# Optimization experiments

Measured on AMD Instinct MI355X. Metric: run time of the kernel, lower is better.

The kernel has to match this reference:

```python
import jax, jax.numpy as jnp
import numpy as np

B, S, E = 2, 2048, 4096
HQ, HKV, D = 32, 8, 128
WINDOW = 1024
SOFT_CAP = 50.0
Q_PRE_ATTN = 128.0
TT_SCALE = 0.1
TT_FLOOR = 8192.0
EPS = 1e-6
ROPE_BASE = 10000.0


def l2norm(x):
    return x * jax.lax.rsqrt(jnp.mean(x * x, axis=-1, keepdims=True) + EPS)


def apply_rope(x, pos):
    # x: [B,S,H,D]; half-split rotary, base 10000
    half = x.shape[-1] // 2
    freq = ROPE_BASE ** (-jnp.arange(half, dtype=jnp.float32) * 2.0 / x.shape[-1])  # [half]
    angle = pos.astype(jnp.float32)[:, None] * freq[None, :]                         # [S,half]
    cos = jnp.cos(angle)[None, :, None, :]
    sin = jnp.sin(angle)[None, :, None, :]
    x1, x2 = x[..., :half], x[..., half:]
    return jnp.concatenate([x1 * cos - x2 * sin, x2 * cos + x1 * sin], axis=-1)


def setup_inputs() -> dict:
    key = jax.random.key(0)
    ks = jax.random.split(key, 5)
    sc = 0.02
    return {
        "x": jax.random.normal(ks[0], (B, S, E), jnp.float32),
        "Wq": jax.random.normal(ks[1], (E, HQ, D), jnp.float32) * sc,
        "Wk": jax.random.normal(ks[2], (E, HKV, D), jnp.float32) * sc,
        "Wv": jax.random.normal(ks[3], (E, HKV, D), jnp.float32) * sc,
        "Wo": jax.random.normal(ks[4], (HQ, D, E), jnp.float32) * sc,
    }


def reference(x, Wq, Wk, Wv, Wo):
    pos = jnp.arange(S)
    # QKV projections
    q = jnp.einsum('bse,ehd->bshd', x, Wq)   # [B,S,HQ,D]
    k = jnp.einsum('bse,ehd->bshd', x, Wk)   # [B,S,HKV,D]
    v = jnp.einsum('bse,ehd->bshd', x, Wv)   # [B,S,HKV,D]
    # QK norm (L2Norm) then RoPE
    q = apply_rope(l2norm(q), pos)
    k = apply_rope(l2norm(k), pos)
    # query pre-attention scaling
    q = q * (Q_PRE_ATTN ** -0.5)
    # temperature tuning: per-position scale
    attn_scale = jnp.log(jnp.floor((pos.astype(jnp.float32) + 1.0) / TT_FLOOR) + 1.0) * TT_SCALE + 1.0
    q = q * attn_scale[None, :, None, None]
    # GQA: expand kv heads
    g = HQ // HKV
    k_r = jnp.repeat(k, g, axis=2)           # [B,S,HQ,D]
    v_r = jnp.repeat(v, g, axis=2)
    logits = jnp.einsum('bihd,bjhd->bhij', q, k_r).astype(jnp.float32)
    # tanh soft cap
    logits = SOFT_CAP * jnp.tanh(logits / SOFT_CAP)
    # causal + sliding window mask: j <= i and i - j < WINDOW
    i = pos[:, None]
    j = pos[None, :]
    mask = (j <= i) & ((i - j) < WINDOW)     # [S,S]
    logits = jnp.where(mask[None, None], logits, jnp.float32(-1e30))
    probs = jax.nn.softmax(logits, axis=-1)
    out = jnp.einsum('bhij,bjhd->bihd', probs, v_r)  # [B,S,HQ,D]
    return jnp.einsum('bihd,hde->bie', out, Wo)      # [B,S,E]
```

## Files before the change

### kernel.cpp

```cpp
#include <hip/hip_runtime.h>


typedef unsigned short u16;
typedef unsigned int   u32;
typedef __bf16 bf16x8 __attribute__((ext_vector_type(8)));
typedef float  f32x4  __attribute__((ext_vector_type(4)));

typedef __attribute__((address_space(1))) void* gas_ptr;
typedef __attribute__((address_space(3))) void* las_ptr;

__device__ __forceinline__ void load_lds16(const void* g, void* l) {
  __builtin_amdgcn_global_load_lds((gas_ptr)g, (las_ptr)l, 16, 0, 0);
}

__device__ __forceinline__ u16 f2bf(float f) {
  u32 u = __builtin_bit_cast(u32, f);
  u += 0x7fffu + ((u >> 16) & 1u);
  return (u16)(u >> 16);
}
__device__ __forceinline__ float bf2f(u16 h) {
  u32 u = ((u32)h) << 16;
  return __builtin_bit_cast(float, u);
}
__device__ __forceinline__ u32 pack_trunc(float a, float b) {
  return (__builtin_bit_cast(u32, a) >> 16) | (__builtin_bit_cast(u32, b) & 0xffff0000u);
}

__global__ __launch_bounds__(256) void cast_f32_bf16(const float* __restrict__ src,
                                                     u16* __restrict__ dst) {
  size_t i = ((size_t)blockIdx.x * 256 + threadIdx.x) * 8;
  float4 a = *(const float4*)(src + i);
  float4 b = *(const float4*)(src + i + 4);
  uint4 o;
  o.x = (u32)f2bf(a.x) | ((u32)f2bf(a.y) << 16);
  o.y = (u32)f2bf(a.z) | ((u32)f2bf(a.w) << 16);
  o.z = (u32)f2bf(b.x) | ((u32)f2bf(b.y) << 16);
  o.w = (u32)f2bf(b.z) | ((u32)f2bf(b.w) << 16);
  *(uint4*)(dst + i) = o;
}

__global__ __launch_bounds__(256) void transpose_cast_f32_bf16(
    const float* __restrict__ src, u16* __restrict__ dst, int R, int C) {
  __shared__ float tile[32][33];
  const int tx = threadIdx.x & 31, ty = threadIdx.x >> 5;
  const int r0 = blockIdx.y * 32, c0 = blockIdx.x * 32;
#pragma unroll
  for (int i = 0; i < 4; ++i)
    tile[ty + i * 8][tx] = src[(size_t)(r0 + ty + i * 8) * C + (c0 + tx)];
  __syncthreads();
  uint2 ov;
  ov.x = (u32)f2bf(tile[ty * 4 + 0][tx]) | ((u32)f2bf(tile[ty * 4 + 1][tx]) << 16);
  ov.y = (u32)f2bf(tile[ty * 4 + 2][tx]) | ((u32)f2bf(tile[ty * 4 + 3][tx]) << 16);
  *(uint2*)&dst[(size_t)(c0 + tx) * R + (r0 + ty * 4)] = ov;
}

__global__ __launch_bounds__(256) void transpose_v(const u16* __restrict__ qkvr,
                                                   u16* __restrict__ vtb) {
  __shared__ u16 tile[32][34];
  const int plane = blockIdx.z;
  const int b = plane >> 3, h8 = plane & 7;
  const u16* s = qkvr + (size_t)(b * 2048) * 6144 + (40 + h8) * 128;
  u16* d = vtb + (size_t)plane * 2048 * 128;
  const int tx = threadIdx.x & 31, ty = threadIdx.x >> 5;
  const int r0 = blockIdx.x * 32, c0 = blockIdx.y * 32;
#pragma unroll
  for (int i = 0; i < 4; ++i)
    tile[ty + i * 8][tx] = s[(size_t)(r0 + ty + i * 8) * 6144 + (c0 + tx)];
  __syncthreads();
  uint2 ov;
  ov.x = (u32)tile[ty * 4 + 0][tx] | ((u32)tile[ty * 4 + 1][tx] << 16);
  ov.y = (u32)tile[ty * 4 + 2][tx] | ((u32)tile[ty * 4 + 3][tx] << 16);
  *(uint2*)&d[(size_t)(c0 + tx) * 2048 + (r0 + ty * 4)] = ov;
}


template <int MB>
__device__ __forceinline__ void mm16(f32x4 (&acc)[8][4], const bf16x8 (&af)[4],
                                     const bf16x8 (&bf)[4]) {
#pragma unroll
  for (int ii = 0; ii < 4; ++ii)
#pragma unroll
    for (int nf = 0; nf < 4; ++nf)
      acc[MB + ii][nf] =
          __builtin_amdgcn_mfma_f32_16x16x32_bf16(af[ii], bf[nf], acc[MB + ii][nf], 0, 0, 0);
}

template <int OUT_BF16>
__global__ __launch_bounds__(512, 2) void gemm256(const u16* __restrict__ A,
                                                  const u16* __restrict__ Bt,
                                                  void* __restrict__ Cout,
                                                  int N, int K, int ntx) {
  __shared__ __align__(16) u16 lds[65536];
  const int t = threadIdx.x, lane = t & 63, w = t >> 6;
  const int c = lane & 15, q = lane >> 4;
  const int wm = w >> 2, wn = w & 3;

  const int cpx = (int)gridDim.x >> 3;
  const int swz = ((int)blockIdx.x & 7) * cpx + ((int)blockIdx.x >> 3);
  const int bx = swz % ntx, by = swz / ntx;
  const int m0 = by << 8, n0 = bx << 8;

  u32 aoff[2][2], boff[2][2];
#pragma unroll
  for (int h = 0; h < 2; ++h)
#pragma unroll
    for (int j = 0; j < 2; ++j) {
      const int rowS = w * 16 + j * 8 + (lane >> 3);
      const int colE = ((lane & 7) ^ (rowS & 7)) * 8;
      aoff[h][j] = (u32)(m0 + h * 128 + rowS) * (u32)K + (u32)colE;
      boff[h][j] = (u32)(n0 + h * 128 + rowS) * (u32)K + (u32)colE;
    }
  const u32 stW = (u32)w * 1024u;

  const u32 sl0 = (u32)((q ^ (c & 7)) * 8);
  const u32 aR = (u32)(wm * 8192 + c * 64) + sl0;
  const u32 bR = (u32)(16384 + (wn >> 1) * 8192 + (wn & 1) * 4096 + c * 64) + sl0;

  f32x4 acc[8][4];
#pragma unroll
  for (int i2 = 0; i2 < 8; ++i2)
#pragma unroll
    for (int j2 = 0; j2 < 4; ++j2) acc[i2][j2] = (f32x4){0.f, 0.f, 0.f, 0.f};

  const int nt = K >> 6;

#define STG_A(bb, hh, kt)                                                \
  do {                                                                   \
    u16* d_ = &lds[(bb) * 32768u + (hh) * 8192u + stW];                  \
    load_lds16(A + (aoff[hh][0] + (u32)(kt) * 64u), d_);                 \
    load_lds16(A + (aoff[hh][1] + (u32)(kt) * 64u), d_ + 512);           \
  } while (0)
#define STG_B(bb, hh, kt)                                                \
  do {                                                                   \
    u16* d_ = &lds[(bb) * 32768u + 16384u + (hh) * 8192u + stW];         \
    load_lds16(Bt + (boff[hh][0] + (u32)(kt) * 64u), d_);                \
    load_lds16(Bt + (boff[hh][1] + (u32)(kt) * 64u), d_ + 512);          \
  } while (0)
#define RD4(dst, base)                                                   \
  do {                                                                   \
    const u16* p_ = &lds[(base)];                                        \
    dst[0] = *(const bf16x8*)(p_);                                       \
    dst[1] = *(const bf16x8*)(p_ + 1024);                                \
    dst[2] = *(const bf16x8*)(p_ + 2048);                                \
    dst[3] = *(const bf16x8*)(p_ + 3072);                                \
  } while (0)
#define BAR __builtin_amdgcn_s_barrier()
#define LGKM0 asm volatile("s_waitcnt lgkmcnt(0)" ::: "memory")
#define LGKM8 asm volatile("s_waitcnt lgkmcnt(8)" ::: "memory")
#define VM6 asm volatile("s_waitcnt vmcnt(6)" ::: "memory")
#define PRIO1 __builtin_amdgcn_s_setprio(1)
#define PRIO0 __builtin_amdgcn_s_setprio(0)

  STG_B(0, 0, 0);
  STG_B(0, 1, 0);
  STG_A(0, 0, 0);
  STG_A(0, 1, 0);
  STG_B(1, 0, 1);
  STG_B(1, 1, 1);
  STG_A(1, 0, 1);
  VM6;
  BAR;

  bf16x8 Bf0[4], Bf1[4], Af0[4], Af1[4];

  for (int i = 0; i < (nt >> 1); ++i) {
    const int tb = 2 * i + 1;
    int t2 = 2 * i + 2; if (t2 >= nt) t2 -= nt;
    int t3 = 2 * i + 3; if (t3 >= nt) t3 -= nt;

    RD4(Bf0, bR);
    RD4(Bf1, bR ^ 32u);
    RD4(Af0, aR);
    STG_A(1, 1, tb);
    LGKM8;
    BAR; LGKM0;
    PRIO1; mm16<0>(acc, Af0, Bf0); PRIO0;
    BAR;
    RD4(Af1, aR + 4096u);
    STG_B(0, 0, t2);
    BAR; LGKM0;
    PRIO1; mm16<4>(acc, Af1, Bf0); PRIO0;
    BAR;
    RD4(Af0, aR ^ 32u);
    RD4(Af1, (aR + 4096u) ^ 32u);
    STG_B(0, 1, t2);
    BAR; LGKM0;
    PRIO1; mm16<0>(acc, Af0, Bf1); PRIO0;
    BAR;
    STG_A(0, 0, t2);
    VM6;
    BAR;
    PRIO1; mm16<4>(acc, Af1, Bf1); PRIO0;
    BAR;

    RD4(Bf0, 32768u + bR);
    RD4(Bf1, (32768u + bR) ^ 32u);
    RD4(Af0, 32768u + aR);
    STG_A(0, 1, t2);
    LGKM8;
    BAR; LGKM0;
    PRIO1; mm16<0>(acc, Af0, Bf0); PRIO0;
    BAR;
    RD4(Af1, 32768u + aR + 4096u);
    STG_B(1, 0, t3);
    BAR; LGKM0;
    PRIO1; mm16<4>(acc, Af1, Bf0); PRIO0;
    BAR;
    RD4(Af0, (32768u + aR) ^ 32u);
    RD4(Af1, (32768u + aR + 4096u) ^ 32u);
    STG_B(1, 1, t3);
    BAR; LGKM0;
    PRIO1; mm16<0>(acc, Af0, Bf1); PRIO0;
    BAR;
    STG_A(1, 0, t3);
    VM6;
    BAR;
    PRIO1; mm16<4>(acc, Af1, Bf1); PRIO0;
    BAR;
  }

  asm volatile("s_waitcnt vmcnt(0)" ::: "memory");

#undef STG_A
#undef STG_B
#undef RD4
#undef BAR
#undef LGKM0
#undef LGKM8
#undef VM6
#undef PRIO1
#undef PRIO0

  const int rb0 = m0 + wm * 128 + q * 4;
  const int cb0 = n0 + wn * 64 + c;
#pragma unroll
  for (int mf = 0; mf < 8; ++mf)
#pragma unroll
    for (int nf = 0; nf < 4; ++nf) {
      const size_t base = (size_t)(rb0 + mf * 16) * N + (cb0 + nf * 16);
#pragma unroll
      for (int r = 0; r < 4; ++r) {
        if (OUT_BF16)
          ((u16*)Cout)[base + (size_t)r * N] = f2bf(acc[mf][nf][r]);
        else
          ((float*)Cout)[base + (size_t)r * N] = acc[mf][nf][r];
      }
    }
}

__global__ __launch_bounds__(256) void qkv_post(const u16* __restrict__ raw,
                                                u16* __restrict__ qb,
                                                u16* __restrict__ kb) {
  const int t = threadIdx.x;
  const int c = t & 15, g = t >> 4;
  const u32 u = (u32)blockIdx.x * 16u + (u32)g;
  const u32 row = u / 40u;
  const int hh = (int)(u - row * 40u);
  const int pos = (int)(row & 2047u);
  const int b = (int)(row >> 11);

  const uint4 rv = *(const uint4*)(raw + (size_t)row * 6144 + hh * 128 + c * 8);
  u32 rw[4] = {rv.x, rv.y, rv.z, rv.w};
  float xs[8];
#pragma unroll
  for (int j = 0; j < 4; ++j) {
    xs[2 * j] = bf2f((u16)(rw[j] & 0xffffu));
    xs[2 * j + 1] = bf2f((u16)(rw[j] >> 16));
  }
  float ss = 0.f;
#pragma unroll
  for (int j = 0; j < 8; ++j) ss += xs[j] * xs[j];
#pragma unroll
  for (int off = 8; off >= 1; off >>= 1) ss += __shfl_xor(ss, off);
  const float rn = rsqrtf(ss * (1.0f / 128.0f) + 1e-6f);

  u32 pw[4];
#pragma unroll
  for (int j = 0; j < 4; ++j) pw[j] = __shfl_xor(rw[j], 8);
  float xp[8];
#pragma unroll
  for (int j = 0; j < 4; ++j) {
    xp[2 * j] = bf2f((u16)(pw[j] & 0xffffu));
    xp[2 * j + 1] = bf2f((u16)(pw[j] >> 16));
  }

  const float sgn = (c < 8) ? -1.0f : 1.0f;
  const int dbase = (c & 7) * 8;
  const float fpos = (float)pos;
  const bool isq = (hh < 32);
  const float sc = (isq ? 0.088388347648318447f : 1.0f) * rn;
  float o[8];
#pragma unroll
  for (int j = 0; j < 8; ++j) {
    const float fr = exp2f(-(float)(dbase + j) * 0.20762050593046f);
    float sn, cs;
    sincosf(fpos * fr, &sn, &cs);
    o[j] = (xs[j] * cs + sgn * xp[j] * sn) * sc;
  }

  uint4 ov;
  ov.x = (u32)f2bf(o[0]) | ((u32)f2bf(o[1]) << 16);
  ov.y = (u32)f2bf(o[2]) | ((u32)f2bf(o[3]) << 16);
  ov.z = (u32)f2bf(o[4]) | ((u32)f2bf(o[5]) << 16);
  ov.w = (u32)f2bf(o[6]) | ((u32)f2bf(o[7]) << 16);
  u16* dst = isq ? (qb + ((size_t)((b * 32 + hh) * 2048 + pos)) * 128)
                 : (kb + ((size_t)((b * 8 + (hh - 32)) * 2048 + pos)) * 128);
  *(uint4*)(dst + c * 8) = ov;
}

__global__ __launch_bounds__(256, 4) void attn_fwd(const u16* __restrict__ qb,
                                                   const u16* __restrict__ kb,
                                                   const u16* __restrict__ vtb,
                                                   u16* __restrict__ attn) {
  __shared__ __align__(16) u16 Ks[64 * 128];
  __shared__ __align__(16) u16 VTs[128 * 64];
  __shared__ __align__(16) u16 Ps[4][16 * 64];

  const int t = threadIdx.x, lane = t & 63, w = t >> 6;
  const int c = lane & 15, quad = lane >> 4;
  const int q0 = blockIdx.x * 64;
  const int bh = blockIdx.y;
  const int b = bh >> 5, hq = bh & 31;
  const int kvp = b * 8 + (hq >> 2);
  const u16* qp = qb + (size_t)bh * (2048 * 128);
  const u16* kp = kb + (size_t)kvp * (2048 * 128);
  const u16* vp = vtb + (size_t)kvp * (128 * 2048);
  u16* Psw = &Ps[w][0];

  bf16x8 qf[4];
  {
    const u16* qrow = qp + (size_t)(q0 + w * 16 + c) * 128 + quad * 8;
#pragma unroll
    for (int ks = 0; ks < 4; ++ks) qf[ks] = *(const bf16x8*)(qrow + ks * 32);
  }

  f32x4 oacc[8];
#pragma unroll
  for (int j = 0; j < 8; ++j)
#pragma unroll
    for (int r = 0; r < 4; ++r) oacc[j][r] = 0.0f;
  float lsum = 0.0f;

  const int i_glob = q0 + w * 16 + c;

  int t0 = q0 - 1023;
  if (t0 < 0) t0 = 0;
  t0 = (t0 >> 6) << 6;

  for (int kv0 = t0; kv0 <= q0; kv0 += 64) {
    __syncthreads();
    {
      const int row_in = lane >> 4, ch = lane & 15;
#pragma unroll
      for (int i = 0; i < 4; ++i) {
        const int row = w * 4 + i * 16 + row_in;
        const int g = ch ^ (row & 15);
        load_lds16(kp + (size_t)(kv0 + row) * 128 + g * 8, &Ks[(w * 4 + i * 16) * 128]);
      }
      const int drow = lane >> 3, ch8 = lane & 7;
#pragma unroll
      for (int i = 0; i < 4; ++i) {
        const int dd = w * 8 + i * 32 + drow;
        const int g = ch8 ^ (dd & 7);
        load_lds16(vp + (size_t)dd * 2048 + kv0 + g * 8, &VTs[(w * 8 + i * 32) * 64]);
      }
    }
    __syncthreads();

    f32x4 sacc[4];
#pragma unroll
    for (int im = 0; im < 4; ++im)
#pragma unroll
      for (int r = 0; r < 4; ++r) sacc[im][r] = 0.0f;

#pragma unroll
    for (int ks = 0; ks < 4; ++ks) {
#pragma unroll
      for (int im = 0; im < 4; ++im) {
        const int key = im * 16 + c;
        const int ch = (ks * 4 + quad) ^ c;
        const bf16x8 af = *(const bf16x8*)&Ks[key * 128 + ch * 8];
        sacc[im] = __builtin_amdgcn_mfma_f32_16x16x32_bf16(af, qf[ks], sacc[im], 0, 0, 0);
      }
    }

    const bool need_mask = (kv0 == q0) || (q0 - kv0 >= 961);
#pragma unroll
    for (int im = 0; im < 4; ++im) {
      float pv[4];
#pragma unroll
      for (int r = 0; r < 4; ++r) {
        const float s = sacc[im][r];
        const float u = s * s;
        const float cap = s * (1.0f + u * (-1.3333333e-4f + u * 2.1333333e-8f));
        pv[r] = __expf(cap);
      }
      if (need_mask) {
        const int j_base = kv0 + im * 16 + quad * 4;
#pragma unroll
        for (int r = 0; r < 4; ++r) {
          const int j_glob = j_base + r;
          if (!((j_glob <= i_glob) && (i_glob - j_glob < 1024))) pv[r] = 0.0f;
        }
      }
      lsum += (pv[0] + pv[1]) + (pv[2] + pv[3]);
      uint2 pk;
      pk.x = pack_trunc(pv[0], pv[1]);
      pk.y = pack_trunc(pv[2], pv[3]);
      *(uint2*)&Psw[c * 64 + ((im * 2 + (quad >> 1)) ^ (c & 7)) * 8 + (quad & 1) * 4] = pk;
    }

#pragma unroll
    for (int ks = 0; ks < 2; ++ks) {
      const bf16x8 pf = *(const bf16x8*)&Psw[c * 64 + ((ks * 4 + quad) ^ (c & 7)) * 8];
#pragma unroll
      for (int jn = 0; jn < 8; ++jn) {
        const int dd = jn * 16 + c;
        const int ch = (ks * 4 + quad) ^ (c & 7);
        const bf16x8 vf = *(const bf16x8*)&VTs[dd * 64 + ch * 8];
        oacc[jn] = __builtin_amdgcn_mfma_f32_16x16x32_bf16(pf, vf, oacc[jn], 0, 0, 0);
      }
    }
  }

  float lt = lsum;
  lt += __shfl_xor(lt, 16);
  lt += __shfl_xor(lt, 32);
  float rl[4];
#pragma unroll
  for (int r = 0; r < 4; ++r)
    rl[r] = __builtin_amdgcn_rcpf(__shfl(lt, quad * 4 + r));

  const size_t obase = ((size_t)(b * 2048 + q0 + w * 16)) * 4096 + hq * 128;
#pragma unroll
  for (int jn = 0; jn < 8; ++jn) {
#pragma unroll
    for (int r = 0; r < 4; ++r) {
      const int q_in = quad * 4 + r;
      attn[obase + (size_t)q_in * 4096 + jn * 16 + c] = f2bf(oacc[jn][r] * rl[r]);
    }
  }
}

extern "C" void kernel_launch(void* const* d_in, const int* in_sizes, int n_in,
                              void* d_out, int out_size, void* d_ws, size_t ws_size,
                              hipStream_t stream) {
  (void)in_sizes; (void)n_in; (void)out_size; (void)ws_size;
  const float* x  = (const float*)d_in[0];
  const float* Wq = (const float*)d_in[1];
  const float* Wk = (const float*)d_in[2];
  const float* Wv = (const float*)d_in[3];
  const float* Wo = (const float*)d_in[4];
  float* out = (float*)d_out;
  char* ws = (char*)d_ws;

  u16* xb    = (u16*)(ws + 0);
  u16* vtb   = (u16*)(ws + 0);
  u16* WqkvT = (u16*)(ws + 33554432ULL);
  u16* qb    = (u16*)(ws + 33554432ULL);
  u16* kb    = (u16*)(ws + 67108864ULL);
  u16* WoT   = (u16*)(ws + 83886080ULL);
  u16* qkvr  = (u16*)(ws + 117440512ULL);
  u16* attnb = (u16*)(ws + 117440512ULL);

  cast_f32_bf16<<<8192, 256, 0, stream>>>(x, xb);
  transpose_cast_f32_bf16<<<dim3(128, 128), 256, 0, stream>>>(Wq, WqkvT, 4096, 4096);
  transpose_cast_f32_bf16<<<dim3(32, 128), 256, 0, stream>>>(Wk, WqkvT + (size_t)4096 * 4096, 4096, 1024);
  transpose_cast_f32_bf16<<<dim3(32, 128), 256, 0, stream>>>(Wv, WqkvT + (size_t)5120 * 4096, 4096, 1024);
  transpose_cast_f32_bf16<<<dim3(128, 128), 256, 0, stream>>>(Wo, WoT, 4096, 4096);

  gemm256<1><<<dim3(384), 512, 0, stream>>>(xb, WqkvT, (void*)qkvr, 6144, 4096, 24);
  qkv_post<<<10240, 256, 0, stream>>>(qkvr, qb, kb);
  transpose_v<<<dim3(64, 4, 16), 256, 0, stream>>>(qkvr, vtb);
  attn_fwd<<<dim3(32, 64), 256, 0, stream>>>(qb, kb, vtb, attnb);
  gemm256<0><<<dim3(256), 512, 0, stream>>>(attnb, WoT, (void*)out, 4096, 4096, 16);
}
```

Baseline: 691.3 us.

## Switch attention to 32x32x16 MFMA with 2x2 warp split over keys and queries

Rewrites the attention inner loop so each wave computes a 32x32 score tile with 32x32x16 bf16 MFMAs. Waves are split two ways over keys and two ways over queries, and the P tile is shared across waves through LDS, which needs an extra block barrier per KV step and a cross-wave row-sum reduction at the end. The goal is higher MFMA efficiency and fewer LDS fragment loads per FLOP. The two transpose kernels also remap threads on the write side so output stores are more contiguous.

```diff
diff --git a/kernel.cpp b/kernel.cpp
--- a/kernel.cpp
+++ b/kernel.cpp
@@ -5,6 +5,7 @@
 typedef unsigned int   u32;
 typedef __bf16 bf16x8 __attribute__((ext_vector_type(8)));
 typedef float  f32x4  __attribute__((ext_vector_type(4)));
+typedef float  f32x16 __attribute__((ext_vector_type(16)));
 
 typedef __attribute__((address_space(1))) void* gas_ptr;
 typedef __attribute__((address_space(3))) void* las_ptr;
@@ -48,10 +49,12 @@
   for (int i = 0; i < 4; ++i)
     tile[ty + i * 8][tx] = src[(size_t)(r0 + ty + i * 8) * C + (c0 + tx)];
   __syncthreads();
+  const int cc = threadIdx.x >> 3;
+  const int rg = threadIdx.x & 7;
   uint2 ov;
-  ov.x = (u32)f2bf(tile[ty * 4 + 0][tx]) | ((u32)f2bf(tile[ty * 4 + 1][tx]) << 16);
-  ov.y = (u32)f2bf(tile[ty * 4 + 2][tx]) | ((u32)f2bf(tile[ty * 4 + 3][tx]) << 16);
-  *(uint2*)&dst[(size_t)(c0 + tx) * R + (r0 + ty * 4)] = ov;
+  ov.x = (u32)f2bf(tile[rg * 4 + 0][cc]) | ((u32)f2bf(tile[rg * 4 + 1][cc]) << 16);
+  ov.y = (u32)f2bf(tile[rg * 4 + 2][cc]) | ((u32)f2bf(tile[rg * 4 + 3][cc]) << 16);
+  *(uint2*)&dst[(size_t)(c0 + cc) * R + (r0 + rg * 4)] = ov;
 }
 
 __global__ __launch_bounds__(256) void transpose_v(const u16* __restrict__ qkvr,
@@ -67,10 +70,12 @@
   for (int i = 0; i < 4; ++i)
     tile[ty + i * 8][tx] = s[(size_t)(r0 + ty + i * 8) * 6144 + (c0 + tx)];
   __syncthreads();
+  const int cc = threadIdx.x >> 3;
+  const int rg = threadIdx.x & 7;
   uint2 ov;
-  ov.x = (u32)tile[ty * 4 + 0][tx] | ((u32)tile[ty * 4 + 1][tx] << 16);
-  ov.y = (u32)tile[ty * 4 + 2][tx] | ((u32)tile[ty * 4 + 3][tx] << 16);
-  *(uint2*)&d[(size_t)(c0 + tx) * 2048 + (r0 + ty * 4)] = ov;
+  ov.x = (u32)tile[rg * 4 + 0][cc] | ((u32)tile[rg * 4 + 1][cc] << 16);
+  ov.y = (u32)tile[rg * 4 + 2][cc] | ((u32)tile[rg * 4 + 3][cc] << 16);
+  *(uint2*)&d[(size_t)(c0 + cc) * 2048 + (r0 + rg * 4)] = ov;
 }
 
 
@@ -314,10 +319,12 @@
                                                    u16* __restrict__ attn) {
   __shared__ __align__(16) u16 Ks[64 * 128];
   __shared__ __align__(16) u16 VTs[128 * 64];
-  __shared__ __align__(16) u16 Ps[4][16 * 64];
+  __shared__ __align__(16) u16 Ps[64 * 64];
+  __shared__ float Ls[2][64];
 
   const int t = threadIdx.x, lane = t & 63, w = t >> 6;
-  const int c = lane & 15, quad = lane >> 4;
+  const int l31 = lane & 31, h5 = lane >> 5;
+  const int kh = w >> 1, qh = w & 1;
   const int q0 = blockIdx.x * 64;
   const int bh = blockIdx.y;
   const int b = bh >> 5, hq = bh & 31;
@@ -325,23 +332,22 @@
   const u16* qp = qb + (size_t)bh * (2048 * 128);
   const u16* kp = kb + (size_t)kvp * (2048 * 128);
   const u16* vp = vtb + (size_t)kvp * (128 * 2048);
-  u16* Psw = &Ps[w][0];
-
-  bf16x8 qf[4];
+
+  bf16x8 qf[8];
   {
-    const u16* qrow = qp + (size_t)(q0 + w * 16 + c) * 128 + quad * 8;
-#pragma unroll
-    for (int ks = 0; ks < 4; ++ks) qf[ks] = *(const bf16x8*)(qrow + ks * 32);
-  }
-
-  f32x4 oacc[8];
-#pragma unroll
-  for (int j = 0; j < 8; ++j)
-#pragma unroll
-    for (int r = 0; r < 4; ++r) oacc[j][r] = 0.0f;
+    const u16* qrow = qp + (size_t)(q0 + qh * 32 + l31) * 128 + h5 * 8;
+#pragma unroll
+    for (int kst = 0; kst < 8; ++kst) qf[kst] = *(const bf16x8*)(qrow + kst * 16);
+  }
+
+  f32x16 oacc[2];
+#pragma unroll
+  for (int dc = 0; dc < 2; ++dc)
+#pragma unroll
+    for (int r = 0; r < 16; ++r) oacc[dc][r] = 0.0f;
   float lsum = 0.0f;
 
-  const int i_glob = q0 + w * 16 + c;
+  const int iq = q0 + qh * 32 + l31;
 
   int t0 = q0 - 1023;
   if (t0 < 0) t0 = 0;
@@ -367,79 +373,92 @@
     }
     __syncthreads();
 
-    f32x4 sacc[4];
-#pragma unroll
-    for (int im = 0; im < 4; ++im)
-#pragma unroll
-      for (int r = 0; r < 4; ++r) sacc[im][r] = 0.0f;
-
-#pragma unroll
-    for (int ks = 0; ks < 4; ++ks) {
-#pragma unroll
-      for (int im = 0; im < 4; ++im) {
-        const int key = im * 16 + c;
-        const int ch = (ks * 4 + quad) ^ c;
-        const bf16x8 af = *(const bf16x8*)&Ks[key * 128 + ch * 8];
-        sacc[im] = __builtin_amdgcn_mfma_f32_16x16x32_bf16(af, qf[ks], sacc[im], 0, 0, 0);
+    f32x16 sacc;
+#pragma unroll
+    for (int r = 0; r < 16; ++r) sacc[r] = 0.0f;
+    {
+      const int key = kh * 32 + l31;
+      const u16* krow = &Ks[key * 128];
+      const int s15 = key & 15;
+#pragma unroll
+      for (int kst = 0; kst < 8; ++kst) {
+        const int phys = (kst * 2 + h5) ^ s15;
+        const bf16x8 af = *(const bf16x8*)(krow + phys * 8);
+        sacc = __builtin_amdgcn_mfma_f32_32x32x16_bf16(af, qf[kst], sacc, 0, 0, 0);
       }
     }
 
     const bool need_mask = (kv0 == q0) || (q0 - kv0 >= 961);
-#pragma unroll
-    for (int im = 0; im < 4; ++im) {
-      float pv[4];
-#pragma unroll
-      for (int r = 0; r < 4; ++r) {
-        const float s = sacc[im][r];
-        const float u = s * s;
-        const float cap = s * (1.0f + u * (-1.3333333e-4f + u * 2.1333333e-8f));
-        pv[r] = __expf(cap);
-      }
-      if (need_mask) {
-        const int j_base = kv0 + im * 16 + quad * 4;
-#pragma unroll
-        for (int r = 0; r < 4; ++r) {
-          const int j_glob = j_base + r;
-          if (!((j_glob <= i_glob) && (i_glob - j_glob < 1024))) pv[r] = 0.0f;
+    float pv[16];
+#pragma unroll
+    for (int r = 0; r < 16; ++r) {
+      const float s = sacc[r];
+      const float u = s * s;
+      const float cap = s * (1.0f + u * (-1.3333333e-4f + u * 2.1333333e-8f));
+      pv[r] = __expf(cap);
+    }
+    if (need_mask) {
+#pragma unroll
+      for (int r = 0; r < 16; ++r) {
+        const int key = kv0 + kh * 32 + (r & 3) + 8 * (r >> 2) + 4 * h5;
+        if (!((key <= iq) && (iq - key < 1024))) pv[r] = 0.0f;
+      }
+    }
+#pragma unroll
+    for (int r = 0; r < 16; ++r) lsum += pv[r];
+
+    {
+      const int qrow = qh * 32 + l31;
+      u16* prow = &Ps[qrow * 64];
+      const int s7 = l31 & 7;
+#pragma unroll
+      for (int g = 0; g < 4; ++g) {
+        uint2 pk;
+        pk.x = pack_trunc(pv[4 * g + 0], pv[4 * g + 1]);
+        pk.y = pack_trunc(pv[4 * g + 2], pv[4 * g + 3]);
+        const int phys = (kh * 4 + g) ^ s7;
+        *(uint2*)(prow + phys * 8 + h5 * 4) = pk;
+      }
+    }
+    __syncthreads();
+
+    {
+      const u16* prow = &Ps[(qh * 32 + l31) * 64];
+      const int s7 = l31 & 7;
+#pragma unroll
+      for (int kst = 0; kst < 4; ++kst) {
+        const int physp = (kst * 2 + h5) ^ s7;
+        const bf16x8 pf = *(const bf16x8*)(prow + physp * 8);
+#pragma unroll
+        for (int dc = 0; dc < 2; ++dc) {
+          const int drow = kh * 64 + dc * 32 + l31;
+          const int physv = (kst * 2 + h5) ^ (drow & 7);
+          const bf16x8 vf = *(const bf16x8*)&VTs[drow * 64 + physv * 8];
+          oacc[dc] = __builtin_amdgcn_mfma_f32_32x32x16_bf16(pf, vf, oacc[dc], 0, 0, 0);
         }
       }
-      lsum += (pv[0] + pv[1]) + (pv[2] + pv[3]);
-      uint2 pk;
-      pk.x = pack_trunc(pv[0], pv[1]);
-      pk.y = pack_trunc(pv[2], pv[3]);
-      *(uint2*)&Psw[c * 64 + ((im * 2 + (quad >> 1)) ^ (c & 7)) * 8 + (quad & 1) * 4] = pk;
-    }
-
-#pragma unroll
-    for (int ks = 0; ks < 2; ++ks) {
-      const bf16x8 pf = *(const bf16x8*)&Psw[c * 64 + ((ks * 4 + quad) ^ (c & 7)) * 8];
-#pragma unroll
-      for (int jn = 0; jn < 8; ++jn) {
-        const int dd = jn * 16 + c;
-        const int ch = (ks * 4 + quad) ^ (c & 7);
-        const bf16x8 vf = *(const bf16x8*)&VTs[dd * 64 + ch * 8];
-        oacc[jn] = __builtin_amdgcn_mfma_f32_16x16x32_bf16(pf, vf, oacc[jn], 0, 0, 0);
-      }
-    }
-  }
-
-  float lt = lsum;
-  lt += __shfl_xor(lt, 16);
-  lt += __shfl_xor(lt, 32);
-  float rl[4];
-#pragma unroll
-  for (int r = 0; r < 4; ++r)
-    rl[r] = __builtin_amdgcn_rcpf(__shfl(lt, quad * 4 + r));
-
-  const size_t obase = ((size_t)(b * 2048 + q0 + w * 16)) * 4096 + hq * 128;
-#pragma unroll
-  for (int jn = 0; jn < 8; ++jn) {
-#pragma unroll
-    for (int r = 0; r < 4; ++r) {
-      const int q_in = quad * 4 + r;
-      attn[obase + (size_t)q_in * 4096 + jn * 16 + c] = f2bf(oacc[jn][r] * rl[r]);
-    }
-  }
+    }
+  }
+
+  float lt = lsum + __shfl_xor(lsum, 32);
+  if (lane < 32) Ls[kh][qh * 32 + lane] = lt;
+  __syncthreads();
+
+  float rl16[16];
+#pragma unroll
+  for (int r = 0; r < 16; ++r) {
+    const int qi = qh * 32 + (r & 3) + 8 * (r >> 2) + 4 * h5;
+    rl16[r] = __builtin_amdgcn_rcpf(Ls[0][qi] + Ls[1][qi]);
+  }
+
+  const size_t ob = ((size_t)(b * 2048 + q0 + qh * 32)) * 4096 + hq * 128 + kh * 64;
+#pragma unroll
+  for (int dc = 0; dc < 2; ++dc)
+#pragma unroll
+    for (int r = 0; r < 16; ++r) {
+      const int qi = (r & 3) + 8 * (r >> 2) + 4 * h5;
+      attn[ob + (size_t)qi * 4096 + dc * 32 + l31] = f2bf(oacc[dc][r] * rl16[r]);
+    }
 }
 
 extern "C" void kernel_launch(void* const* d_in, const int* in_sizes, int n_in,
```

Measured after the change: 691.4 us. Within noise of the previous version (+0.0%).

## Load K/V fragments directly from global memory per wave and coalesce transpose stores

Applied to the files above, without the earlier changes.

The attention kernel stops staging K and V tiles in shared memory. Each wave now reads its MFMA operand fragments straight from global memory and iterates over its own 16-query range, so the block-level barriers go away and each wave has its own loop bound and mask test. The two transpose kernels remap threads so that adjacent threads write adjacent rows, which is meant to make the global stores better coalesced. The cost is that K/V reuse across the four waves now depends on the cache rather than LDS, with more global traffic and latency exposed to the MFMA loop.

```diff
diff --git a/kernel.cpp b/kernel.cpp
--- a/kernel.cpp
+++ b/kernel.cpp
@@ -48,10 +48,12 @@
   for (int i = 0; i < 4; ++i)
     tile[ty + i * 8][tx] = src[(size_t)(r0 + ty + i * 8) * C + (c0 + tx)];
   __syncthreads();
+  const int cc = threadIdx.x >> 3;
+  const int rg = threadIdx.x & 7;
   uint2 ov;
-  ov.x = (u32)f2bf(tile[ty * 4 + 0][tx]) | ((u32)f2bf(tile[ty * 4 + 1][tx]) << 16);
-  ov.y = (u32)f2bf(tile[ty * 4 + 2][tx]) | ((u32)f2bf(tile[ty * 4 + 3][tx]) << 16);
-  *(uint2*)&dst[(size_t)(c0 + tx) * R + (r0 + ty * 4)] = ov;
+  ov.x = (u32)f2bf(tile[rg * 4 + 0][cc]) | ((u32)f2bf(tile[rg * 4 + 1][cc]) << 16);
+  ov.y = (u32)f2bf(tile[rg * 4 + 2][cc]) | ((u32)f2bf(tile[rg * 4 + 3][cc]) << 16);
+  *(uint2*)&dst[(size_t)(c0 + cc) * R + (r0 + rg * 4)] = ov;
 }
 
 __global__ __launch_bounds__(256) void transpose_v(const u16* __restrict__ qkvr,
@@ -67,10 +69,12 @@
   for (int i = 0; i < 4; ++i)
     tile[ty + i * 8][tx] = s[(size_t)(r0 + ty + i * 8) * 6144 + (c0 + tx)];
   __syncthreads();
+  const int cc = threadIdx.x >> 3;
+  const int rg = threadIdx.x & 7;
   uint2 ov;
-  ov.x = (u32)tile[ty * 4 + 0][tx] | ((u32)tile[ty * 4 + 1][tx] << 16);
-  ov.y = (u32)tile[ty * 4 + 2][tx] | ((u32)tile[ty * 4 + 3][tx] << 16);
-  *(uint2*)&d[(size_t)(c0 + tx) * 2048 + (r0 + ty * 4)] = ov;
+  ov.x = (u32)tile[rg * 4 + 0][cc] | ((u32)tile[rg * 4 + 1][cc] << 16);
+  ov.y = (u32)tile[rg * 4 + 2][cc] | ((u32)tile[rg * 4 + 3][cc] << 16);
+  *(uint2*)&d[(size_t)(c0 + cc) * 2048 + (r0 + rg * 4)] = ov;
 }
 
 
@@ -312,13 +316,11 @@
                                                    const u16* __restrict__ kb,
                                                    const u16* __restrict__ vtb,
                                                    u16* __restrict__ attn) {
-  __shared__ __align__(16) u16 Ks[64 * 128];
-  __shared__ __align__(16) u16 VTs[128 * 64];
   __shared__ __align__(16) u16 Ps[4][16 * 64];
 
   const int t = threadIdx.x, lane = t & 63, w = t >> 6;
   const int c = lane & 15, quad = lane >> 4;
-  const int q0 = blockIdx.x * 64;
+  const int q0 = blockIdx.x * 64 + w * 16;
   const int bh = blockIdx.y;
   const int b = bh >> 5, hq = bh & 31;
   const int kvp = b * 8 + (hq >> 2);
@@ -329,7 +331,7 @@
 
   bf16x8 qf[4];
   {
-    const u16* qrow = qp + (size_t)(q0 + w * 16 + c) * 128 + quad * 8;
+    const u16* qrow = qp + (size_t)(q0 + c) * 128 + quad * 8;
 #pragma unroll
     for (int ks = 0; ks < 4; ++ks) qf[ks] = *(const bf16x8*)(qrow + ks * 32);
   }
@@ -341,32 +343,14 @@
     for (int r = 0; r < 4; ++r) oacc[j][r] = 0.0f;
   float lsum = 0.0f;
 
-  const int i_glob = q0 + w * 16 + c;
+  const int iq = q0 + c;
 
   int t0 = q0 - 1023;
   if (t0 < 0) t0 = 0;
   t0 = (t0 >> 6) << 6;
-
-  for (int kv0 = t0; kv0 <= q0; kv0 += 64) {
-    __syncthreads();
-    {
-      const int row_in = lane >> 4, ch = lane & 15;
-#pragma unroll
-      for (int i = 0; i < 4; ++i) {
-        const int row = w * 4 + i * 16 + row_in;
-        const int g = ch ^ (row & 15);
-        load_lds16(kp + (size_t)(kv0 + row) * 128 + g * 8, &Ks[(w * 4 + i * 16) * 128]);
-      }
-      const int drow = lane >> 3, ch8 = lane & 7;
-#pragma unroll
-      for (int i = 0; i < 4; ++i) {
-        const int dd = w * 8 + i * 32 + drow;
-        const int g = ch8 ^ (dd & 7);
-        load_lds16(vp + (size_t)dd * 2048 + kv0 + g * 8, &VTs[(w * 8 + i * 32) * 64]);
-      }
-    }
-    __syncthreads();
-
+  const int kvmax = ((q0 + 15) >> 6) << 6;
+
+  for (int kv0 = t0; kv0 <= kvmax; kv0 += 64) {
     f32x4 sacc[4];
 #pragma unroll
     for (int im = 0; im < 4; ++im)
@@ -377,14 +361,13 @@
     for (int ks = 0; ks < 4; ++ks) {
 #pragma unroll
       for (int im = 0; im < 4; ++im) {
-        const int key = im * 16 + c;
-        const int ch = (ks * 4 + quad) ^ c;
-        const bf16x8 af = *(const bf16x8*)&Ks[key * 128 + ch * 8];
+        const bf16x8 af = *(const bf16x8*)(kp + (size_t)(kv0 + im * 16 + c) * 128 +
+                                           (ks * 4 + quad) * 8);
         sacc[im] = __builtin_amdgcn_mfma_f32_16x16x32_bf16(af, qf[ks], sacc[im], 0, 0, 0);
       }
     }
 
-    const bool need_mask = (kv0 == q0) || (q0 - kv0 >= 961);
+    const bool need_mask = (kv0 + 63 > q0) || (kv0 + 1008 < q0);
 #pragma unroll
     for (int im = 0; im < 4; ++im) {
       float pv[4];
@@ -400,7 +383,7 @@
 #pragma unroll
         for (int r = 0; r < 4; ++r) {
           const int j_glob = j_base + r;
-          if (!((j_glob <= i_glob) && (i_glob - j_glob < 1024))) pv[r] = 0.0f;
+          if (!((j_glob <= iq) && (iq - j_glob < 1024))) pv[r] = 0.0f;
         }
       }
       lsum += (pv[0] + pv[1]) + (pv[2] + pv[3]);
@@ -415,9 +398,8 @@
       const bf16x8 pf = *(const bf16x8*)&Psw[c * 64 + ((ks * 4 + quad) ^ (c & 7)) * 8];
 #pragma unroll
       for (int jn = 0; jn < 8; ++jn) {
-        const int dd = jn * 16 + c;
-        const int ch = (ks * 4 + quad) ^ (c & 7);
-        const bf16x8 vf = *(const bf16x8*)&VTs[dd * 64 + ch * 8];
+        const bf16x8 vf = *(const bf16x8*)(vp + (size_t)(jn * 16 + c) * 2048 + kv0 +
+                                           (ks * 4 + quad) * 8);
         oacc[jn] = __builtin_amdgcn_mfma_f32_16x16x32_bf16(pf, vf, oacc[jn], 0, 0, 0);
       }
     }
@@ -431,7 +413,7 @@
   for (int r = 0; r < 4; ++r)
     rl[r] = __builtin_amdgcn_rcpf(__shfl(lt, quad * 4 + r));
 
-  const size_t obase = ((size_t)(b * 2048 + q0 + w * 16)) * 4096 + hq * 128;
+  const size_t obase = ((size_t)(b * 2048 + q0)) * 4096 + hq * 128;
 #pragma unroll
   for (int jn = 0; jn < 8; ++jn) {
 #pragma unroll
```

Result: slower. 1.070 ms (+54.7%).
